# Kernel tuning notes

Measured on AMD Instinct MI355X. Metric: run time of the kernel, lower is better.

The kernel has to match this reference:

```python
import jax, jax.numpy as jnp
from jax import lax
import numpy as np

EPS = 1e-5

def sign_ste(x):
    # Binarize to {-1,+1} with straight-through estimator (matches BNN Binarize)
    return x + lax.stop_gradient(jnp.where(x >= 0, 1.0, -1.0).astype(x.dtype) - x)

def bn(x, g, b, m, v, axis):
    shp = [1] * x.ndim
    shp[axis] = -1
    inv = g.reshape(shp) / jnp.sqrt(v.reshape(shp) + EPS)
    return (x - m.reshape(shp)) * inv + b.reshape(shp)

def bconv(x, w, b, p):
    # binarized-weight conv, NCHW / OIHW
    y = lax.conv_general_dilated(x, sign_ste(w), (1, 1), [(p, p), (p, p)],
                                 dimension_numbers=('NCHW', 'OIHW', 'NCHW'))
    return y + b[None, :, None, None]

def conv_block(x, w, b, g, bt, m, v, p):
    # BinarizeConv2d -> BatchNorm2d(eval) -> Hardtanh -> Quantizer(1 bit)
    return sign_ste(jnp.clip(bn(bconv(x, w, b, p), g, bt, m, v, 1), -1.0, 1.0))

def maxpool2(x):
    return lax.reduce_window(x, -jnp.inf, lax.max, (1, 1, 2, 2), (1, 1, 2, 2), 'VALID')


def setup_inputs() -> dict:
    key = jax.random.key(0)
    ks = iter(jax.random.split(key, 64))
    B = 4096
    d = {}
    d['x'] = jax.random.normal(next(ks), (B, 1, 28, 28), dtype=jnp.float32)

    def u(shape):
        return jax.random.uniform(next(ks), shape, minval=-1.0, maxval=1.0, dtype=jnp.float32)

    def bn_params(c, pre):
        d[pre + 'g'] = u((c,)) * 0.5 + 1.0
        d[pre + 'bt'] = u((c,)) * 0.1
        d[pre + 'm'] = u((c,)) * 0.1
        d[pre + 'v'] = jax.random.uniform(next(ks), (c,), minval=0.5, maxval=1.5, dtype=jnp.float32)

    # stem conv 1->16, k=3
    d['w1'] = u((16, 1, 3, 3)); d['b1'] = jnp.full((16,), 0.01, jnp.float32); bn_params(16, '')
    d['g1'], d['bt1'], d['m1'], d['v1'] = d.pop('g'), d.pop('bt'), d.pop('m'), d.pop('v')
    # inception branches 16->32 each
    d['wa'] = u((32, 16, 1, 1)); d['ba'] = jnp.full((32,), 0.01, jnp.float32); bn_params(32, 'a_')
    d['wb'] = u((32, 16, 3, 3)); d['bb'] = jnp.full((32,), 0.01, jnp.float32); bn_params(32, 'b_')
    d['wc'] = u((32, 16, 5, 5)); d['bc'] = jnp.full((32,), 0.01, jnp.float32); bn_params(32, 'c_')
    # classifier
    d['wf1'] = u((1024, 7 * 7 * 3 * 32)); d['bf1'] = jnp.full((1024,), 0.01, jnp.float32); bn_params(1024, 'f1_')
    d['wf2'] = u((10, 1024)); d['bf2'] = jnp.full((10,), 0.01, jnp.float32); bn_params(10, 'f2_')
    return d


def reference(x, w1, b1, g1, bt1, m1, v1,
              wa, ba, a_g, a_bt, a_m, a_v,
              wb, bb, b_g, b_bt, b_m, b_v,
              wc, bc, c_g, c_bt, c_m, c_v,
              wf1, bf1, f1_g, f1_bt, f1_m, f1_v,
              wf2, bf2, f2_g, f2_bt, f2_m, f2_v):
    h = conv_block(x, w1, b1, g1, bt1, m1, v1, 1)          # [B,16,28,28]
    h = maxpool2(h)                                         # [B,16,14,14]
    h = sign_ste(h)  # BinarizeConv2d binarizes its input (>1 channel); no-op on +/-1
    ya = conv_block(h, wa, ba, a_g, a_bt, a_m, a_v, 0)
    yb = conv_block(h, wb, bb, b_g, b_bt, b_m, b_v, 1)
    yc = conv_block(h, wc, bc, c_g, c_bt, c_m, c_v, 2)
    h = jnp.concatenate([ya, yb, yc], axis=1)               # [B,96,14,14]
    h = maxpool2(h)                                         # [B,96,7,7]
    h = h.reshape(h.shape[0], -1)                           # [B,4704] (NCHW flatten)
    # fc1: binarized input + binarized weights, BN1d, hardtanh, quantize
    h = sign_ste(h) @ sign_ste(wf1).T + bf1
    h = sign_ste(jnp.clip(bn(h, f1_g, f1_bt, f1_m, f1_v, 1), -1.0, 1.0))
    # dropout is identity in eval mode
    h = sign_ste(h) @ sign_ste(wf2).T + bf2
    h = bn(h, f2_g, f2_bt, f2_m, f2_v, 1)
    return jax.nn.log_softmax(h, axis=-1)                   # [B,10]
```

## Files before the change

kernel.cpp:

```cpp
#include <hip/hip_runtime.h>
#include <stdint.h>

typedef unsigned long long u64;
typedef unsigned int u32;
typedef unsigned short u16;

struct InPtrs { const float* p[37]; };

#define OFF_THR1     0
#define OFF_W1D      128
#define OFF_WREC     1280
#define OFF_SMAXBC   4352
#define OFF_SMAXF1   11008
#define OFF_WF2P     15104
#define OFF_A2       16384
#define OFF_C2       16448
#define OFF_WF1P     16512
#define OFF_H2       622720
#define OFF_HB2      3047552

__device__ __forceinline__ int clampi(int v, int lo, int hi) { return v < lo ? lo : (v > hi ? hi : v); }

__global__ __launch_bounds__(1024) void kprep(InPtrs P, char* __restrict__ ws) {
  const float* w1 = P.p[1]; const float* b1 = P.p[2];
  const float* g1 = P.p[3]; const float* bt1 = P.p[4]; const float* m1 = P.p[5]; const float* v1 = P.p[6];
  const float* wa = P.p[7]; const float* ba = P.p[8];
  const float* ag = P.p[9]; const float* abt = P.p[10]; const float* am = P.p[11]; const float* av = P.p[12];
  const float* wb = P.p[13]; const float* bb = P.p[14];
  const float* bg = P.p[15]; const float* bbt = P.p[16]; const float* bm = P.p[17]; const float* bv = P.p[18];
  const float* wc = P.p[19]; const float* bc = P.p[20];
  const float* bf1 = P.p[26];
  const float* f1g = P.p[27]; const float* f1bt = P.p[28]; const float* f1m = P.p[29]; const float* f1v = P.p[30];
  const float* wf2 = P.p[31]; const float* bf2 = P.p[32];
  const float* cg = P.p[21]; const float* cbt = P.p[22]; const float* cm = P.p[23]; const float* cv = P.p[24];
  const float* f2g = P.p[33]; const float* f2bt = P.p[34]; const float* f2m = P.p[35]; const float* f2v = P.p[36];

  double* thr1 = (double*)(ws + OFF_THR1);
  double* w1d  = (double*)(ws + OFF_W1D);
  u64* wrec = (u64*)(ws + OFF_WREC);
  u64* smaxbc = (u64*)(ws + OFF_SMAXBC);
  int* smf1 = (int*)(ws + OFF_SMAXF1);
  u64* wf2p = (u64*)(ws + OFF_WF2P);
  float* a2 = (float*)(ws + OFF_A2);
  float* c2 = (float*)(ws + OFF_C2);

  __shared__ u64 wbpL[96];
  __shared__ u64 wcpL[256];
  __shared__ double thBL[32], thCL[32];
  __shared__ u32 wamS[32], smaS[32];

  int t = threadIdx.x;
  int wave = t >> 6, lane = t & 63;

  if (t < 144) w1d[t] = (w1[t] >= 0.f) ? 1.0 : -1.0;
  if (t < 16) {
    double inv = (double)g1[t] / sqrt((double)v1[t] + 1e-5);
    thr1[t] = (double)m1[t] - (double)bt1[t] / inv - (double)b1[t];
  }
  if (t < 32) {
    u32 m = 0;
    for (int c = 0; c < 16; c++) if (wa[t*16+c] >= 0.f) m |= 1u << c;
    wamS[t] = m;
    double ia = (double)ag[t] / sqrt((double)av[t] + 1e-5);
    double thA = (double)am[t] - (double)abt[t]/ia - (double)ba[t];
    int kmin = (int)ceil(thA);
    int sm = (16 - kmin) >> 1;
    smaS[t] = (u32)clampi(sm + 1, 0, 65535);
    double ib = (double)bg[t] / sqrt((double)bv[t] + 1e-5);
    thBL[t] = (double)bm[t] - (double)bbt[t]/ib - (double)bb[t];
    double ic = (double)cg[t] / sqrt((double)cv[t] + 1e-5);
    thCL[t] = (double)cm[t] - (double)cbt[t]/ic - (double)bc[t];
  }
  for (int w = wave; w < 96; w += 16) {
    int ch = w / 3, k = w - 3*ch;
    int tt = 4*k + (lane >> 4), c = lane & 15;
    bool pred = false;
    if (tt < 9) pred = (wb[ch*144 + c*9 + tt] >= 0.f);
    u64 m = __ballot(pred);
    if (lane == 0) wbpL[w] = m;
  }
  for (int w = wave; w < 256; w += 16) {
    int ch = w >> 3, k = w & 7;
    int tt = 4*k + (lane >> 4), c = lane & 15;
    bool pred = false;
    if (k < 7 && tt < 25) pred = (wc[ch*400 + c*25 + tt] >= 0.f);
    u64 m = __ballot(pred);
    if (lane == 0) wcpL[w] = m;
  }
  for (int w = wave; w < 160; w += 16) {
    int o = w >> 4, kk = w & 15;
    bool pred = (wf2[o*1024 + kk*64 + lane] >= 0.f);
    u64 m = __ballot(pred);
    if (lane == 0) wf2p[w] = m;
  }
  if (t < 10) {
    double inv = (double)f2g[t] / sqrt((double)f2v[t] + 1e-5);
    a2[t] = (float)inv;
    c2[t] = (float)(((double)bf2[t] - (double)f2m[t]) * inv + (double)f2bt[t]);
  }
  {
    int o = t;
    double inv = (double)f1g[o] / sqrt((double)f1v[o] + 1e-5);
    double th = (double)f1m[o] - (double)f1bt[o]/inv - (double)bf1[o];
    int kmin = (int)ceil(th);
    smf1[o] = ((4704 - kmin) >> 1) + 1;
  }
  __syncthreads();
  if (t < 384) {
    int ch = t / 12, k = t - 12*ch;
    u64 v = 0;
    if (k < 7) v = wcpL[ch*8 + k];
    else if (k < 10) v = wbpL[ch*3 + (k - 7)];
    wrec[ch*12 + k] = v;
  }
  if (t < 800) {
    const int irep[5] = {0, 1, 5, 12, 13};
    int cls = t >> 5, ch = t & 31;
    int rc = cls / 5, cc = cls - 5*rc;
    int ir = irep[rc], jr = irep[cc];
    u64 invC[7] = {0,0,0,0,0,0,0};
    u64 invB[3] = {0,0,0};
    int nInvC = 0, nInvB = 0;
    #pragma unroll
    for (int tt = 0; tt < 25; tt++) {
      int di = tt/5 - 2, dj = tt%5 - 2;
      bool val = (ir+di >= 0 && ir+di < 14 && jr+dj >= 0 && jr+dj < 14);
      if (!val) { invC[tt>>2] |= 0xFFFFull << ((tt&3)*16); nInvC++; }
    }
    #pragma unroll
    for (int tt = 0; tt < 9; tt++) {
      int di = tt/3 - 1, dj = tt%3 - 1;
      bool val = (ir+di >= 0 && ir+di < 14 && jr+dj >= 0 && jr+dj < 14);
      if (!val) { invB[tt>>2] |= 0xFFFFull << ((tt&3)*16); nInvB++; }
    }
    int pinvC = 0;
    #pragma unroll
    for (int k = 0; k < 7; k++) pinvC += __popcll(wcpL[ch*8+k] & invC[k]);
    int pinvB = 0;
    #pragma unroll
    for (int k = 0; k < 3; k++) pinvB += __popcll(wbpL[ch*3+k] & invB[k]);
    int nvC = 16*(25 - nInvC), nvB = 16*(9 - nInvB);
    int kminC = (int)ceil(thCL[ch]);
    int kminB = (int)ceil(thBL[ch]);
    int smC = ((nvC - kminC) >> 1) + pinvC;
    int smB = ((nvB - kminB) >> 1) + pinvB;
    u64 pB = (u64)clampi(smB + 1, 0, 65535);
    u64 pC = (u64)clampi(smC + 1, 0, 65535);
    smaxbc[cls*33 + ch] = ((u64)wamS[ch] << 48) | ((u64)smaS[ch] << 32) | (pB << 16) | pC;
  }
}

__global__ __launch_bounds__(256) void kpackwf1(const float* __restrict__ wf1, u64* __restrict__ wf1p) {
  __shared__ unsigned char flag[4704];
  int o = blockIdx.x, t = threadIdx.x;
  const float* row = wf1 + (size_t)o*4704;
  for (int i = t; i < 4704; i += 256) flag[i] = (row[i] >= 0.f);
  __syncthreads();
  int w0 = t >> 6, lane = t & 63;
  for (int w = w0; w < 74; w += 4) {
    int fp = w*64 + lane;
    bool bit = false;
    if (fp < 4704) { int s = fp / 96, c = fp - 96*s; bit = flag[c*49 + s] != 0; }
    u64 m = __ballot(bit);
    if (lane == 0) wf1p[(size_t)o*74 + w] = m;
  }
}

__global__ __launch_bounds__(256) void kfused(const float* __restrict__ x, const char* __restrict__ ws,
                                              u32* __restrict__ h2u32) {
  __shared__ float wshF[144];
  __shared__ float thrF[16];
  __shared__ double thrD[16];
  __shared__ u16 hp[324];
  __shared__ u32 rr[196][3];
  __shared__ u64 smbc[825];
  __shared__ __align__(16) u64 wrecL[384];

  const double* w1d  = (const double*)(ws + OFF_W1D);
  const double* thr1 = (const double*)(ws + OFF_THR1);
  const u64* wrec_g = (const u64*)(ws + OFF_WREC);
  const u64* smaxbc_g = (const u64*)(ws + OFF_SMAXBC);

  int t = threadIdx.x, b = blockIdx.x;
  if (t < 144) wshF[t] = (float)w1d[t];
  else if (t < 160) { thrF[t-144] = (float)thr1[t-144]; thrD[t-144] = thr1[t-144]; }
  for (int i = t; i < 384; i += 256) wrecL[i] = wrec_g[i];
  for (int i = t; i < 825; i += 256) smbc[i] = smaxbc_g[i];
  {
    u32* hp32 = (u32*)hp;
    for (int i = t; i < 162; i += 256) hp32[i] = 0;
  }
  __syncthreads();

  int pi = t / 14, pj = t - 14*pi;
  if (t < 196) {
    const float* xi = x + (size_t)b*784;
    float p[16];
    #pragma unroll
    for (int r = 0; r < 4; r++) {
      int ii = 2*pi - 1 + r;
      #pragma unroll
      for (int c = 0; c < 4; c++) {
        int jj = 2*pj - 1 + c;
        bool v = (ii >= 0 && ii < 28 && jj >= 0 && jj < 28);
        int a = v ? (ii*28 + jj) : 0;
        float f = xi[a];
        p[r*4+c] = v ? f : 0.0f;
      }
    }
    u32 bits = 0;
    for (int o = 0; o < 16; o++) {
      float a00 = 0.f, a01 = 0.f, a10 = 0.f, a11 = 0.f;
      #pragma unroll
      for (int dy = 0; dy < 3; dy++)
        #pragma unroll
        for (int dx = 0; dx < 3; dx++) {
          float w = wshF[o*9 + dy*3 + dx];
          a00 += p[dy*4 + dx]       * w;
          a01 += p[dy*4 + dx + 1]   * w;
          a10 += p[(dy+1)*4 + dx]   * w;
          a11 += p[(dy+1)*4 + dx+1] * w;
        }
      float th = thrF[o];
      float m0 = fminf(fabsf(a00 - th), fabsf(a01 - th));
      float m1 = fminf(fabsf(a10 - th), fabsf(a11 - th));
      bool bit;
      if (fminf(m0, m1) < 5e-4f) {
        double d00 = 0.0, d01 = 0.0, d10 = 0.0, d11 = 0.0;
        #pragma unroll
        for (int dy = 0; dy < 3; dy++)
          #pragma unroll
          for (int dx = 0; dx < 3; dx++) {
            double w = (double)wshF[o*9 + dy*3 + dx];
            d00 += (double)p[dy*4 + dx]       * w;
            d01 += (double)p[dy*4 + dx + 1]   * w;
            d10 += (double)p[(dy+1)*4 + dx]   * w;
            d11 += (double)p[(dy+1)*4 + dx+1] * w;
          }
        double thd = thrD[o];
        bit = (d00 >= thd) || (d01 >= thd) || (d10 >= thd) || (d11 >= thd);
      } else {
        bit = (a00 >= th) || (a01 >= th) || (a10 >= th) || (a11 >= th);
      }
      bits |= (u32)bit << o;
    }
    hp[(pi+2)*18 + (pj+2)] = (u16)bits;
  }
  __syncthreads();

  if (t < 196) {
    const u16* hpb = &hp[pi*18 + pj];
    u32 tp[25];
    #pragma unroll
    for (int r = 0; r < 5; r++)
      #pragma unroll
      for (int c = 0; c < 5; c++) tp[r*5+c] = hpb[r*18 + c];
    u32 h0 = tp[12];
    u64 qc[6], qb[2];
    u32 qc6 = tp[24], qb2 = tp[18];
    qc[0] = (u64)tp[0]  | (u64)tp[1]<<16  | (u64)tp[2]<<32  | (u64)tp[3]<<48;
    qc[1] = (u64)tp[4]  | (u64)tp[5]<<16  | (u64)tp[6]<<32  | (u64)tp[7]<<48;
    qc[2] = (u64)tp[8]  | (u64)tp[9]<<16  | (u64)tp[10]<<32 | (u64)tp[11]<<48;
    qc[3] = (u64)tp[12] | (u64)tp[13]<<16 | (u64)tp[14]<<32 | (u64)tp[15]<<48;
    qc[4] = (u64)tp[16] | (u64)tp[17]<<16 | (u64)tp[18]<<32 | (u64)tp[19]<<48;
    qc[5] = (u64)tp[20] | (u64)tp[21]<<16 | (u64)tp[22]<<32 | (u64)tp[23]<<48;
    qb[0] = (u64)tp[6]  | (u64)tp[7]<<16  | (u64)tp[8]<<32  | (u64)tp[11]<<48;
    qb[1] = (u64)tp[12] | (u64)tp[13]<<16 | (u64)tp[16]<<32 | (u64)tp[17]<<48;
    int rc = (pi < 2) ? pi : (pi > 11 ? pi - 9 : 2);
    int cc = (pj < 2) ? pj : (pj > 11 ? pj - 9 : 2);
    const u64* mrow = &smbc[(rc*5 + cc)*33];
    const ulonglong2* R2 = (const ulonglong2*)wrecL;
    u32 r0 = 0, r1 = 0, r2 = 0;
    #pragma unroll 8
    for (int ch = 0; ch < 32; ch++) {
      ulonglong2 w01 = R2[ch*6+0], w23 = R2[ch*6+1], w45 = R2[ch*6+2];
      ulonglong2 w67 = R2[ch*6+3], w89 = R2[ch*6+4];
      u64 meta = mrow[ch];
      int Sc = __popcll(qc[0]^w01.x) + __popcll(qc[1]^w01.y) + __popcll(qc[2]^w23.x)
             + __popcll(qc[3]^w23.y) + __popcll(qc[4]^w45.x) + __popcll(qc[5]^w45.y)
             + __popc(qc6 ^ (u32)w67.x);
      int Sb = __popcll(qb[0]^w67.y) + __popcll(qb[1]^w89.x) + __popc(qb2 ^ (u32)w89.y);
      int Sa = __popc(h0 ^ (u32)(meta >> 48));
      r0 |= (u32)(Sa < (int)((meta >> 32) & 0xFFFFu)) << ch;
      r1 |= (u32)(Sb < (int)((meta >> 16) & 0xFFFFu)) << ch;
      r2 |= (u32)(Sc < (int)(meta & 0xFFFFu)) << ch;
    }
    rr[t][0] = r0; rr[t][1] = r1; rr[t][2] = r2;
  }
  __syncthreads();
  if (t < 148) {
    u32 v = 0;
    if (t < 147) {
      int s = t / 3, qq = t - 3*s;
      int sp = s / 7, sj = s - 7*sp;
      int base = (2*sp)*14 + 2*sj;
      v = rr[base][qq] | rr[base+1][qq] | rr[base+14][qq] | rr[base+15][qq];
    }
    h2u32[(size_t)b*148 + t] = v;
  }
}

__global__ __launch_bounds__(256) void kfc1(const u64* __restrict__ h2, const u64* __restrict__ wf1p,
                                            const int* __restrict__ smf1, u64* __restrict__ hb2) {
  __shared__ __align__(16) u64 aL[64*74];
  __shared__ __align__(16) u64 wL[64*74];
  __shared__ unsigned char bitsb[64][64];
  int bx = blockIdx.x, by = blockIdx.y, t = threadIdx.x;
  const ulonglong2* ga = reinterpret_cast<const ulonglong2*>(h2 + (size_t)by*(64*74));
  ulonglong2* la = reinterpret_cast<ulonglong2*>(aL);
  for (int i = t; i < 64*37; i += 256) la[i] = ga[i];
  const ulonglong2* gw = reinterpret_cast<const ulonglong2*>(wf1p + (size_t)bx*(64*74));
  ulonglong2* lw = reinterpret_cast<ulonglong2*>(wL);
  for (int i = t; i < 64*37; i += 256) {
    int o = i / 37, w2 = i - 37*o;
    int po = ((o & 15) << 2) | (o >> 4);
    lw[po*37 + w2] = gw[i];
  }
  __syncthreads();
  int ig = t & 15, og = t >> 4;
  const ulonglong2* A0 = reinterpret_cast<const ulonglong2*>(aL + (ig     )*74);
  const ulonglong2* A1 = reinterpret_cast<const ulonglong2*>(aL + (ig + 16)*74);
  const ulonglong2* A2 = reinterpret_cast<const ulonglong2*>(aL + (ig + 32)*74);
  const ulonglong2* A3 = reinterpret_cast<const ulonglong2*>(aL + (ig + 48)*74);
  const ulonglong2* W0 = reinterpret_cast<const ulonglong2*>(wL + (og*4 + 0)*74);
  const ulonglong2* W1 = reinterpret_cast<const ulonglong2*>(wL + (og*4 + 1)*74);
  const ulonglong2* W2 = reinterpret_cast<const ulonglong2*>(wL + (og*4 + 2)*74);
  const ulonglong2* W3 = reinterpret_cast<const ulonglong2*>(wL + (og*4 + 3)*74);
  int s[4][4];
  #pragma unroll
  for (int i = 0; i < 4; i++)
    #pragma unroll
    for (int j = 0; j < 4; j++) s[i][j] = 0;
  for (int w = 0; w < 37; w++) {
    ulonglong2 b0 = W0[w], b1 = W1[w], b2 = W2[w], b3 = W3[w];
    ulonglong2 a;
    a = A0[w];
    s[0][0] += __popcll(a.x^b0.x)+__popcll(a.y^b0.y); s[0][1] += __popcll(a.x^b1.x)+__popcll(a.y^b1.y);
    s[0][2] += __popcll(a.x^b2.x)+__popcll(a.y^b2.y); s[0][3] += __popcll(a.x^b3.x)+__popcll(a.y^b3.y);
    a = A1[w];
    s[1][0] += __popcll(a.x^b0.x)+__popcll(a.y^b0.y); s[1][1] += __popcll(a.x^b1.x)+__popcll(a.y^b1.y);
    s[1][2] += __popcll(a.x^b2.x)+__popcll(a.y^b2.y); s[1][3] += __popcll(a.x^b3.x)+__popcll(a.y^b3.y);
    a = A2[w];
    s[2][0] += __popcll(a.x^b0.x)+__popcll(a.y^b0.y); s[2][1] += __popcll(a.x^b1.x)+__popcll(a.y^b1.y);
    s[2][2] += __popcll(a.x^b2.x)+__popcll(a.y^b2.y); s[2][3] += __popcll(a.x^b3.x)+__popcll(a.y^b3.y);
    a = A3[w];
    s[3][0] += __popcll(a.x^b0.x)+__popcll(a.y^b0.y); s[3][1] += __popcll(a.x^b1.x)+__popcll(a.y^b1.y);
    s[3][2] += __popcll(a.x^b2.x)+__popcll(a.y^b2.y); s[3][3] += __popcll(a.x^b3.x)+__popcll(a.y^b3.y);
  }
  int th0 = smf1[bx*64 + og];
  int th1 = smf1[bx*64 + og + 16];
  int th2 = smf1[bx*64 + og + 32];
  int th3 = smf1[bx*64 + og + 48];
  #pragma unroll
  for (int i = 0; i < 4; i++) {
    int im = ig + 16*i;
    bitsb[im][og     ] = s[i][0] < th0;
    bitsb[im][og + 16] = s[i][1] < th1;
    bitsb[im][og + 32] = s[i][2] < th2;
    bitsb[im][og + 48] = s[i][3] < th3;
  }
  __syncthreads();
  if (t < 64) {
    u64 wd = 0;
    #pragma unroll
    for (int j = 0; j < 64; j++) wd |= (u64)bitsb[t][j] << j;
    hb2[(size_t)(by*64 + t)*16 + bx] = wd;
  }
}

__global__ __launch_bounds__(256) void kfc2(const u64* __restrict__ hb2, const char* __restrict__ ws,
                                            float* __restrict__ out, int B) {
  __shared__ u64 w2[160];
  __shared__ float a2s[10], c2s[10];
  const u64* wf2p = (const u64*)(ws + OFF_WF2P);
  const float* a2 = (const float*)(ws + OFF_A2);
  const float* c2 = (const float*)(ws + OFF_C2);
  int t = threadIdx.x;
  for (int i = t; i < 160; i += 256) w2[i] = wf2p[i];
  if (t < 10) { a2s[t] = a2[t]; c2s[t] = c2[t]; }
  __syncthreads();
  int img = blockIdx.x*256 + t;
  if (img >= B) return;
  u64 a[16];
  #pragma unroll
  for (int w = 0; w < 16; w++) a[w] = hb2[(size_t)img*16 + w];
  float z[10];
  #pragma unroll
  for (int o = 0; o < 10; o++) {
    int S = 0;
    #pragma unroll
    for (int w = 0; w < 16; w++) S += __popcll(a[w] ^ w2[o*16 + w]);
    z[o] = (float)(1024 - 2*S) * a2s[o] + c2s[o];
  }
  float M = z[0];
  #pragma unroll
  for (int o = 1; o < 10; o++) M = fmaxf(M, z[o]);
  float se = 0.f;
  #pragma unroll
  for (int o = 0; o < 10; o++) se += expf(z[o] - M);
  float lse = M + logf(se);
  #pragma unroll
  for (int o = 0; o < 10; o++) out[(size_t)img*10 + o] = z[o] - lse;
}

extern "C" void kernel_launch(void* const* d_in, const int* in_sizes, int n_in,
                              void* d_out, int out_size, void* d_ws, size_t ws_size,
                              hipStream_t stream) {
  int B = in_sizes[0] / 784;
  char* ws = (char*)d_ws;
  InPtrs P;
  for (int i = 0; i < 37; i++) P.p[i] = (const float*)d_in[i];

  kprep<<<1, 1024, 0, stream>>>(P, ws);
  kpackwf1<<<1024, 256, 0, stream>>>((const float*)d_in[25], (u64*)(ws + OFF_WF1P));
  kfused<<<B, 256, 0, stream>>>((const float*)d_in[0], ws, (u32*)(ws + OFF_H2));
  dim3 g(16, B/64);
  kfc1<<<g, 256, 0, stream>>>((const u64*)(ws + OFF_H2), (const u64*)(ws + OFF_WF1P),
                              (const int*)(ws + OFF_SMAXF1), (u64*)(ws + OFF_HB2));
  kfc2<<<(B + 255)/256, 256, 0, stream>>>((const u64*)(ws + OFF_HB2), ws, (float*)d_out, B);
}
```

Before: 151.4 us.

## Process five images per block in fused conv kernel and simplify pool threshold test

```diff
diff --git a/kernel.cpp b/kernel.cpp
--- a/kernel.cpp
+++ b/kernel.cpp
@@ -18,6 +18,8 @@
 #define OFF_WF1P     16512
 #define OFF_H2       622720
 #define OFF_HB2      3047552
+
+#define IMGS 5
 
 __device__ __forceinline__ int clampi(int v, int lo, int hi) { return v < lo ? lo : (v > hi ? hi : v); }
 
@@ -166,13 +168,13 @@
   }
 }
 
-__global__ __launch_bounds__(256) void kfused(const float* __restrict__ x, const char* __restrict__ ws,
-                                              u32* __restrict__ h2u32) {
+__global__ __launch_bounds__(512) void kfused(const float* __restrict__ x, const char* __restrict__ ws,
+                                              u32* __restrict__ h2u32, int B) {
   __shared__ float wshF[144];
   __shared__ float thrF[16];
   __shared__ double thrD[16];
-  __shared__ u16 hp[324];
-  __shared__ u32 rr[196][3];
+  __shared__ u16 hp[IMGS*324];
+  __shared__ u32 rr[IMGS*196][3];
   __shared__ u64 smbc[825];
   __shared__ __align__(16) u64 wrecL[384];
 
@@ -182,19 +184,23 @@
   const u64* smaxbc_g = (const u64*)(ws + OFF_SMAXBC);
 
   int t = threadIdx.x, b = blockIdx.x;
+  int img0 = b * IMGS;
+  int nimg = B - img0; if (nimg > IMGS) nimg = IMGS;
   if (t < 144) wshF[t] = (float)w1d[t];
   else if (t < 160) { thrF[t-144] = (float)thr1[t-144]; thrD[t-144] = thr1[t-144]; }
-  for (int i = t; i < 384; i += 256) wrecL[i] = wrec_g[i];
-  for (int i = t; i < 825; i += 256) smbc[i] = smaxbc_g[i];
+  for (int i = t; i < 384; i += 512) wrecL[i] = wrec_g[i];
+  for (int i = t; i < 825; i += 512) smbc[i] = smaxbc_g[i];
   {
     u32* hp32 = (u32*)hp;
-    for (int i = t; i < 162; i += 256) hp32[i] = 0;
-  }
-  __syncthreads();
-
-  int pi = t / 14, pj = t - 14*pi;
-  if (t < 196) {
-    const float* xi = x + (size_t)b*784;
+    for (int i = t; i < IMGS*162; i += 512) hp32[i] = 0;
+  }
+  __syncthreads();
+
+  for (int task = t; task < nimg*196; task += 512) {
+    int img = task / 196;
+    int px  = task - 196*img;
+    int pi = px / 14, pj = px - 14*pi;
+    const float* xi = x + (size_t)(img0 + img)*784;
     float p[16];
     #pragma unroll
     for (int r = 0; r < 4; r++) {
@@ -222,10 +228,9 @@
           a11 += p[(dy+1)*4 + dx+1] * w;
         }
       float th = thrF[o];
-      float m0 = fminf(fabsf(a00 - th), fabsf(a01 - th));
-      float m1 = fminf(fabsf(a10 - th), fabsf(a11 - th));
+      float mx = fmaxf(fmaxf(a00, a01), fmaxf(a10, a11));
       bool bit;
-      if (fminf(m0, m1) < 5e-4f) {
+      if (fabsf(mx - th) < 5e-4f) {
         double d00 = 0.0, d01 = 0.0, d10 = 0.0, d11 = 0.0;
         #pragma unroll
         for (int dy = 0; dy < 3; dy++)
@@ -240,16 +245,19 @@
         double thd = thrD[o];
         bit = (d00 >= thd) || (d01 >= thd) || (d10 >= thd) || (d11 >= thd);
       } else {
-        bit = (a00 >= th) || (a01 >= th) || (a10 >= th) || (a11 >= th);
+        bit = (mx >= th);
       }
       bits |= (u32)bit << o;
     }
-    hp[(pi+2)*18 + (pj+2)] = (u16)bits;
-  }
-  __syncthreads();
-
-  if (t < 196) {
-    const u16* hpb = &hp[pi*18 + pj];
+    hp[img*324 + (pi+2)*18 + (pj+2)] = (u16)bits;
+  }
+  __syncthreads();
+
+  for (int task = t; task < nimg*196; task += 512) {
+    int img = task / 196;
+    int px  = task - 196*img;
+    int pi = px / 14, pj = px - 14*pi;
+    const u16* hpb = &hp[img*324 + pi*18 + pj];
     u32 tp[25];
     #pragma unroll
     for (int r = 0; r < 5; r++)
@@ -285,18 +293,19 @@
       r1 |= (u32)(Sb < (int)((meta >> 16) & 0xFFFFu)) << ch;
       r2 |= (u32)(Sc < (int)(meta & 0xFFFFu)) << ch;
     }
-    rr[t][0] = r0; rr[t][1] = r1; rr[t][2] = r2;
-  }
-  __syncthreads();
-  if (t < 148) {
+    rr[task][0] = r0; rr[task][1] = r1; rr[task][2] = r2;
+  }
+  __syncthreads();
+  for (int task = t; task < nimg*148; task += 512) {
+    int im = task / 148, q = task - 148*im;
     u32 v = 0;
-    if (t < 147) {
-      int s = t / 3, qq = t - 3*s;
+    if (q < 147) {
+      int s = q / 3, qq = q - 3*s;
       int sp = s / 7, sj = s - 7*sp;
-      int base = (2*sp)*14 + 2*sj;
+      int base = im*196 + (2*sp)*14 + 2*sj;
       v = rr[base][qq] | rr[base+1][qq] | rr[base+14][qq] | rr[base+15][qq];
     }
-    h2u32[(size_t)b*148 + t] = v;
+    h2u32[(size_t)(img0+im)*148 + q] = v;
   }
 }
 
@@ -413,7 +422,7 @@
 
   kprep<<<1, 1024, 0, stream>>>(P, ws);
   kpackwf1<<<1024, 256, 0, stream>>>((const float*)d_in[25], (u64*)(ws + OFF_WF1P));
-  kfused<<<B, 256, 0, stream>>>((const float*)d_in[0], ws, (u32*)(ws + OFF_H2));
+  kfused<<<(B + IMGS - 1)/IMGS, 512, 0, stream>>>((const float*)d_in[0], ws, (u32*)(ws + OFF_H2), B);
   dim3 g(16, B/64);
   kfc1<<<g, 256, 0, stream>>>((const u64*)(ws + OFF_H2), (const u64*)(ws + OFF_WF1P),
                               (const int*)(ws + OFF_SMAXF1), (u64*)(ws + OFF_HB2));
```

Measured after the change: 154.3 us. About the same (+1.9%).
